# Performance work log

Measured on AMD Instinct MI355X. Metric: run time of the kernel, lower is better.

## Reference

```python
import jax, jax.numpy as jnp
import numpy as np

N, C, H, DH = 4096, 256, 8, 32
E = 32768
MAX_SPD = 3
DEG_B = 8
LN_EPS = 1e-5


def _ln(h, g, b):
    mu = jnp.mean(h, axis=-1, keepdims=True)
    var = jnp.mean((h - mu) ** 2, axis=-1, keepdims=True)
    return g * (h - mu) / jnp.sqrt(var + LN_EPS) + b


def setup_inputs() -> dict:
    key = jax.random.key(0)
    ks = jax.random.split(key, 16)
    s = 1.0 / np.sqrt(C).astype(np.float32)
    s4 = 1.0 / np.sqrt(4 * C).astype(np.float32)
    return {
        "x": jax.random.normal(ks[0], (N, C), jnp.float32),
        "edge_index": jax.random.randint(ks[1], (2, E), 0, N, dtype=jnp.int32),
        "Wq": jax.random.normal(ks[2], (C, C), jnp.float32) * s,
        "bq": jnp.zeros((C,), jnp.float32),
        "Wk": jax.random.normal(ks[3], (C, C), jnp.float32) * s,
        "bk": jnp.zeros((C,), jnp.float32),
        "Wv": jax.random.normal(ks[4], (C, C), jnp.float32) * s,
        "bv": jnp.zeros((C,), jnp.float32),
        "Wo": jax.random.normal(ks[5], (C, C), jnp.float32) * s,
        "bo": jnp.zeros((C,), jnp.float32),
        "W1": jax.random.normal(ks[6], (C, 4 * C), jnp.float32) * s,
        "b1": jnp.zeros((4 * C,), jnp.float32),
        "W2": jax.random.normal(ks[7], (4 * C, C), jnp.float32) * s4,
        "b2": jnp.zeros((C,), jnp.float32),
        "g1": jnp.ones((C,), jnp.float32),
        "beta1": jnp.zeros((C,), jnp.float32),
        "g2": jnp.ones((C,), jnp.float32),
        "beta2": jnp.zeros((C,), jnp.float32),
        # spd_emb is zero-init in torch; use small random so the bias path is exercised
        "spd_emb": jax.random.normal(ks[8], (MAX_SPD + 2, H), jnp.float32) * 0.02,
        "in_deg_emb": jax.random.normal(ks[9], (DEG_B + 1, C), jnp.float32) * 0.02,
        "out_deg_emb": jax.random.normal(ks[10], (DEG_B + 1, C), jnp.float32) * 0.02,
        "et_bias": jax.random.normal(ks[11], (), jnp.float32) * 0.02,
    }


def _bucket(d):
    # floor(log2(d+1)) clamped to [0, DEG_B]
    return jnp.clip(jnp.floor(jnp.log2(d + 1.0)), 0, DEG_B).astype(jnp.int32)


def _spd_buckets(src, dst):
    # use_reverse_spd=True: adjacency A[row=dst, col=src]; anchors = dst, probe = src.
    # Frontier F starts as identity over all nodes (superset of unique-anchor columns;
    # extra columns never probed -> identical result to torch's unique-anchor version).
    F = jnp.eye(N, dtype=jnp.float32)
    spd = jnp.full((E,), MAX_SPD + 1, dtype=jnp.int32)
    unset = jnp.ones((E,), dtype=bool)
    for k in range(1, MAX_SPD + 1):
        # (A @ F) > 0  via edge-gather + per-row max (binary reachability)
        F = (jax.ops.segment_max(F[src], dst, num_segments=N) > 0).astype(jnp.float32)
        reach = F[src, dst] > 0  # probe anchor column dst at row src
        newly = unset & reach
        spd = jnp.where(newly, k, spd)
        unset = unset & ~newly
    return jnp.clip(spd, 1, MAX_SPD + 1)


def reference(x, edge_index, Wq, bq, Wk, bk, Wv, bv, Wo, bo, W1, b1, W2, b2,
              g1, beta1, g2, beta2, spd_emb, in_deg_emb, out_deg_emb, et_bias):
    src, dst = edge_index[0], edge_index[1]
    ones = jnp.ones((E,), jnp.float32)
    in_deg = jax.ops.segment_sum(ones, dst, num_segments=N)
    out_deg = jax.ops.segment_sum(ones, src, num_segments=N)
    x_in = x + in_deg_emb[_bucket(in_deg)] + out_deg_emb[_bucket(out_deg)]

    spd = _spd_buckets(src, dst)  # [E] int in [1, MAX_SPD+1]

    xn = _ln(x_in, g1, beta1)
    Q = (xn @ Wq + bq).reshape(N, H, DH)
    K = (xn @ Wk + bk).reshape(N, H, DH)
    V = (xn @ Wv + bv).reshape(N, H, DH)

    scores = jnp.sum(Q[dst] * K[src], axis=-1) / np.sqrt(DH)  # [E, H]
    scores = scores + spd_emb[spd] + et_bias

    # segment softmax over edges sharing a destination node
    m = jax.ops.segment_max(scores, dst, num_segments=N)  # [N, H]
    m = jnp.where(jnp.isfinite(m), m, 0.0)
    e = jnp.exp(scores - m[dst])
    ssum = jax.ops.segment_sum(e, dst, num_segments=N)
    w = e / jnp.where(ssum[dst] > 0, ssum[dst], 1.0)  # [E, H]

    msg = jax.ops.segment_sum(w[:, :, None] * V[src], dst, num_segments=N)  # [N,H,DH]
    h = x_in + msg.reshape(N, C) @ Wo + bo
    hn = _ln(h, g2, beta2)
    ff = jax.nn.gelu(hn @ W1 + b1, approximate=False) @ W2 + b2
    return h + ff
```

## Files before the change

kernel.cpp:

```cpp
#include <hip/hip_runtime.h>
#include <math.h>

#define NN 4096
#define CC 256
#define HH 8
#define DHD 32
#define EE 32768
#define FW 128
#define MAXD 64

typedef float f32x4 __attribute__((ext_vector_type(4)));
typedef __bf16 bf16x8 __attribute__((ext_vector_type(8)));
typedef __bf16 bf16x4 __attribute__((ext_vector_type(4)));

__device__ __forceinline__ int bucketf(int d){
  float l = log2f((float)d + 1.0f);
  int b = (int)floorf(l);
  return b < 0 ? 0 : (b > 8 ? 8 : b);
}

__global__ void k_scatter(const int* __restrict__ src, const int* __restrict__ dst,
                          int* __restrict__ cursor, int* __restrict__ outdeg,
                          int* __restrict__ nsrc){
  int e = blockIdx.x*256+threadIdx.x;
  if(e<EE){
    int d = dst[e], s = src[e];
    atomicAdd(&outdeg[s],1);
    int p = atomicAdd(&cursor[d],1);
    if(p < MAXD) nsrc[d*MAXD+p] = s;
  }
}

__global__ void k_mid(const int* __restrict__ cursor, const int* __restrict__ nsrc,
                      unsigned* __restrict__ F1,
                      const float* __restrict__ x,
                      const int* __restrict__ outdeg, const float* __restrict__ iemb,
                      const float* __restrict__ oemb, const float* __restrict__ g,
                      const float* __restrict__ be, float* __restrict__ x_in,
                      __bf16* __restrict__ xn){
  int b = blockIdx.x;
  int tid = threadIdx.x;
  if(b < 2048){
    int d = b*2 + (tid>>7);
    int w = tid & 127;
    int cdeg = cursor[d]; if(cdeg > MAXD) cdeg = MAXD;
    const int* row = nsrc + d*MAXD;
    unsigned v = 0;
    for(int i=0;i<cdeg;i++){
      int s = row[i];
      if((s>>5) == w) v |= 1u << (s&31);
    }
    F1[(size_t)d*FW + w] = v;
    return;
  }
  int node = (b-2048)*4 + (tid >> 6);
  int lane = tid & 63;
  int bi = bucketf(cursor[node]);
  int bo = bucketf(outdeg[node]);
  float4 xv = ((const float4*)(x + (size_t)node*CC))[lane];
  float4 iv = ((const float4*)(iemb + (size_t)bi*CC))[lane];
  float4 ov = ((const float4*)(oemb + (size_t)bo*CC))[lane];
  float4 v;
  v.x = xv.x+iv.x+ov.x; v.y = xv.y+iv.y+ov.y;
  v.z = xv.z+iv.z+ov.z; v.w = xv.w+iv.w+ov.w;
  ((float4*)(x_in + (size_t)node*CC))[lane] = v;
  float s  = v.x+v.y+v.z+v.w;
  float sq = v.x*v.x+v.y*v.y+v.z*v.z+v.w*v.w;
  #pragma unroll
  for(int m=32;m>=1;m>>=1){ s += __shfl_xor(s,m); sq += __shfl_xor(sq,m); }
  float mu  = s * (1.0f/CC);
  float var = sq * (1.0f/CC) - mu*mu;
  float inv = rsqrtf(var + 1e-5f);
  float4 gv = ((const float4*)g)[lane];
  float4 bv = ((const float4*)be)[lane];
  bf16x4 o;
  o[0] = (__bf16)(gv.x*(v.x-mu)*inv + bv.x);
  o[1] = (__bf16)(gv.y*(v.y-mu)*inv + bv.y);
  o[2] = (__bf16)(gv.z*(v.z-mu)*inv + bv.z);
  o[3] = (__bf16)(gv.w*(v.w-mu)*inv + bv.w);
  *(bf16x4*)(xn + (size_t)node*CC + lane*4) = o;
}

__global__ void k_prop(const int* __restrict__ cursor, const int* __restrict__ nsrc,
                       const unsigned* __restrict__ Fin, unsigned* __restrict__ Fout){
  int d = blockIdx.x; int w = threadIdx.x;
  int cdeg = cursor[d]; if(cdeg > MAXD) cdeg = MAXD;
  const int* row = nsrc + d*MAXD;
  unsigned v = 0;
  for(int i=0;i<cdeg;i++){
    v |= Fin[(size_t)row[i]*FW + w];
  }
  Fout[(size_t)d*FW + w] = v;
}

__global__ void k_pre(const float* __restrict__ Wq, const float* __restrict__ Wk,
                      const float* __restrict__ Wv, const float* __restrict__ Wo,
                      const float* __restrict__ W1, const float* __restrict__ W2,
                      const float* __restrict__ bq, const float* __restrict__ bk,
                      const float* __restrict__ bv,
                      __bf16* __restrict__ WqkvT, __bf16* __restrict__ WoT,
                      __bf16* __restrict__ W1T, __bf16* __restrict__ W2T,
                      float* __restrict__ bqkv, int* __restrict__ zero_base){
  int b = blockIdx.x;
  int tid = threadIdx.x;
  if(b >= 193){
    zero_base[(b-193)*256 + tid] = 0;
    return;
  }
  if(b == 192){
    bqkv[tid]     = bq[tid];
    bqkv[256+tid] = bk[tid];
    bqkv[512+tid] = bv[tid];
    return;
  }
  const float* W; __bf16* Wt; int K, N, tile;
  if(b < 16)      { W=Wq; Wt=WqkvT;        K=256;  N=256;  tile=b; }
  else if(b < 32) { W=Wk; Wt=WqkvT+65536;  K=256;  N=256;  tile=b-16; }
  else if(b < 48) { W=Wv; Wt=WqkvT+131072; K=256;  N=256;  tile=b-32; }
  else if(b < 64) { W=Wo; Wt=WoT;          K=256;  N=256;  tile=b-48; }
  else if(b < 128){ W=W1; Wt=W1T;          K=256;  N=1024; tile=b-64; }
  else            { W=W2; Wt=W2T;          K=1024; N=256;  tile=b-128; }
  int nK = K/64;
  int tk = tile % nK, tn = tile / nK;
  __shared__ float T[64][65];
  int c = tid & 63, r0 = tid >> 6;
  #pragma unroll
  for(int i=0;i<16;i++){
    int row = r0*16 + i;
    T[row][c] = W[(size_t)(tk*64+row)*N + tn*64 + c];
  }
  __syncthreads();
  #pragma unroll
  for(int i=0;i<16;i++){
    int row = r0*16 + i;
    Wt[(size_t)(tn*64+row)*K + tk*64 + c] = (__bf16)T[c][row];
  }
}

template<int MODE>
__global__ __launch_bounds__(256) void k_bgemm(const __bf16* __restrict__ A, const __bf16* __restrict__ Bt,
                       const float* __restrict__ bias, const float* __restrict__ add,
                       float* __restrict__ outf, __bf16* __restrict__ outb,
                       int M, int N, int K){
  __shared__ __bf16 As[64*64];
  __shared__ __bf16 Bs[64*64];
  const int tid = threadIdx.x;
  const int lane = tid & 63;
  const int w = tid >> 6;
  const int wr = w >> 1, wc = w & 1;
  const int l15 = lane & 15, g = lane >> 4;
  const int bm = blockIdx.y*64, bn = blockIdx.x*64;
  f32x4 acc[2][2] = {};
  for(int k0=0; k0<K; k0+=64){
    #pragma unroll
    for(int rep=0; rep<2; rep++){
      int q = tid + rep*256;
      int row = q>>3;
      int scb = ((q&7)*16) ^ ((row&7)<<4);
      const __bf16* srcA = A  + (size_t)(bm+row)*K + k0 + (scb>>1);
      const __bf16* srcB = Bt + (size_t)(bn+row)*K + k0 + (scb>>1);
      __builtin_amdgcn_global_load_lds(
        (const __attribute__((address_space(1))) void*)srcA,
        (__attribute__((address_space(3))) void*)((char*)As + q*16), 16, 0, 0);
      __builtin_amdgcn_global_load_lds(
        (const __attribute__((address_space(1))) void*)srcB,
        (__attribute__((address_space(3))) void*)((char*)Bs + q*16), 16, 0, 0);
    }
    __syncthreads();
    #pragma unroll
    for(int ks=0; ks<2; ks++){
      bf16x8 a[2], b[2];
      #pragma unroll
      for(int i=0;i<2;i++){
        int row = wr*32 + i*16 + l15;
        int byte_ = row*128 + ks*64 + g*16; byte_ ^= (row&7)<<4;
        a[i] = *(const bf16x8*)((const char*)As + byte_);
      }
      #pragma unroll
      for(int j=0;j<2;j++){
        int row = wc*32 + j*16 + l15;
        int byte_ = row*128 + ks*64 + g*16; byte_ ^= (row&7)<<4;
        b[j] = *(const bf16x8*)((const char*)Bs + byte_);
      }
      #pragma unroll
      for(int i=0;i<2;i++)
        #pragma unroll
        for(int j=0;j<2;j++)
          acc[i][j] = __builtin_amdgcn_mfma_f32_16x16x32_bf16(a[i], b[j], acc[i][j], 0, 0, 0);
    }
    __syncthreads();
  }
  #pragma unroll
  for(int i=0;i<2;i++){
    #pragma unroll
    for(int j=0;j<2;j++){
      int col = bn + wc*32 + j*16 + l15;
      float bv = bias[col];
      #pragma unroll
      for(int r=0;r<4;r++){
        int rowg = bm + wr*32 + i*16 + g*4 + r;
        float v = acc[i][j][r] + bv;
        if(MODE==1) v += add[(size_t)rowg*N + col];
        if(MODE==2){
          v = 0.5f*v*(1.0f + erff(v*0.70710678118654752f));
          outb[(size_t)rowg*N + col] = (__bf16)v;
        } else if(MODE==3){
          outb[(size_t)rowg*N + col] = (__bf16)v;
        } else {
          outf[(size_t)rowg*N + col] = v;
        }
      }
    }
  }
}

__global__ __launch_bounds__(256) void k_wln(const __bf16* __restrict__ A, const __bf16* __restrict__ Bt,
                    const float* __restrict__ bias, const float* __restrict__ add,
                    const float* __restrict__ g2, const float* __restrict__ be2,
                    float* __restrict__ hbuf, __bf16* __restrict__ hn){
  __shared__ __bf16 As[16*64];
  __shared__ __bf16 Bs[256*64];
  __shared__ float partS[64], partQ[64], muv[16], invv[16];
  const int tid = threadIdx.x;
  const int lane = tid & 63;
  const int w = tid >> 6;
  const int l15 = lane & 15, g = lane >> 4;
  const int bm = blockIdx.x*16;
  const int K = 256, N = 256;
  f32x4 acc[4] = {};
  for(int k0=0; k0<K; k0+=64){
    if(tid < 128){
      int q = tid;
      int row = q>>3;
      int scb = ((q&7)*16) ^ ((row&7)<<4);
      const __bf16* srcA = A + (size_t)(bm+row)*K + k0 + (scb>>1);
      __builtin_amdgcn_global_load_lds(
        (const __attribute__((address_space(1))) void*)srcA,
        (__attribute__((address_space(3))) void*)((char*)As + q*16), 16, 0, 0);
    }
    #pragma unroll
    for(int rep=0; rep<8; rep++){
      int q = tid + rep*256;
      int row = q>>3;
      int scb = ((q&7)*16) ^ ((row&7)<<4);
      const __bf16* srcB = Bt + (size_t)row*K + k0 + (scb>>1);
      __builtin_amdgcn_global_load_lds(
        (const __attribute__((address_space(1))) void*)srcB,
        (__attribute__((address_space(3))) void*)((char*)Bs + q*16), 16, 0, 0);
    }
    __syncthreads();
    #pragma unroll
    for(int ks=0; ks<2; ks++){
      bf16x8 a, b[4];
      { int row = l15;
        int byte_ = row*128 + ks*64 + g*16; byte_ ^= (row&7)<<4;
        a = *(const bf16x8*)((const char*)As + byte_); }
      #pragma unroll
      for(int j=0;j<4;j++){
        int row = w*64 + j*16 + l15;
        int byte_ = row*128 + ks*64 + g*16; byte_ ^= (row&7)<<4;
        b[j] = *(const bf16x8*)((const char*)Bs + byte_);
      }
      #pragma unroll
      for(int j=0;j<4;j++)
        acc[j] = __builtin_amdgcn_mfma_f32_16x16x32_bf16(a, b[j], acc[j], 0, 0, 0);
    }
    __syncthreads();
  }
  float v[4][4];
  #pragma unroll
  for(int j=0;j<4;j++){
    int col = w*64 + j*16 + l15;
    float bv = bias[col];
    #pragma unroll
    for(int r=0;r<4;r++){
      int rowg = bm + g*4 + r;
      v[j][r] = acc[j][r] + bv + add[(size_t)rowg*N + col];
    }
  }
  float s[4], qq[4];
  #pragma unroll
  for(int r=0;r<4;r++){
    s[r] = v[0][r]+v[1][r]+v[2][r]+v[3][r];
    qq[r] = v[0][r]*v[0][r]+v[1][r]*v[1][r]+v[2][r]*v[2][r]+v[3][r]*v[3][r];
  }
  #pragma unroll
  for(int m=8;m>=1;m>>=1){
    #pragma unroll
    for(int r=0;r<4;r++){ s[r] += __shfl_xor(s[r],m); qq[r] += __shfl_xor(qq[r],m); }
  }
  if(l15==0){
    #pragma unroll
    for(int r=0;r<4;r++){ partS[w*16 + g*4 + r] = s[r]; partQ[w*16 + g*4 + r] = qq[r]; }
  }
  __syncthreads();
  if(tid < 16){
    float S = partS[tid] + partS[16+tid] + partS[32+tid] + partS[48+tid];
    float Q = partQ[tid] + partQ[16+tid] + partQ[32+tid] + partQ[48+tid];
    float mu = S * (1.0f/256.0f);
    float var = Q * (1.0f/256.0f) - mu*mu;
    muv[tid] = mu;
    invv[tid] = rsqrtf(var + 1e-5f);
  }
  __syncthreads();
  #pragma unroll
  for(int j=0;j<4;j++){
    int col = w*64 + j*16 + l15;
    float gv = g2[col], bev = be2[col];
    #pragma unroll
    for(int r=0;r<4;r++){
      int rowg = bm + g*4 + r;
      float mu = muv[g*4+r], iv = invv[g*4+r];
      hbuf[(size_t)rowg*N + col] = v[j][r];
      hn[(size_t)rowg*N + col] = (__bf16)(gv*(v[j][r]-mu)*iv + bev);
    }
  }
}

__global__ __launch_bounds__(256) void k_pq(const int* __restrict__ cursor, const int* __restrict__ nsrc,
                    const unsigned* __restrict__ F2, unsigned* __restrict__ F3,
                    const __bf16* __restrict__ A, const __bf16* __restrict__ Bt,
                    const float* __restrict__ bias, __bf16* __restrict__ outb){
  __shared__ __bf16 As[64*64];
  __shared__ __bf16 Bs[64*64];
  const int b = blockIdx.x;
  const int tid = threadIdx.x;
  if(b < 2048){
    int d = b*2 + (tid>>7);
    int w_ = tid & 127;
    int cdeg = cursor[d]; if(cdeg > MAXD) cdeg = MAXD;
    const int* row = nsrc + d*MAXD;
    unsigned v = 0;
    for(int i=0;i<cdeg;i++) v |= F2[(size_t)row[i]*FW + w_];
    F3[(size_t)d*FW + w_] = v;
    return;
  }
  const int bx = b - 2048;
  const int N = 768, K = 256;
  const int bm = (bx/12)*64, bn = (bx%12)*64;
  const int lane = tid & 63;
  const int w = tid >> 6;
  const int wr = w >> 1, wc = w & 1;
  const int l15 = lane & 15, g = lane >> 4;
  f32x4 acc[2][2] = {};
  for(int k0=0; k0<K; k0+=64){
    #pragma unroll
    for(int rep=0; rep<2; rep++){
      int q = tid + rep*256;
      int row = q>>3;
      int scb = ((q&7)*16) ^ ((row&7)<<4);
      const __bf16* srcA = A  + (size_t)(bm+row)*K + k0 + (scb>>1);
      const __bf16* srcB = Bt + (size_t)(bn+row)*K + k0 + (scb>>1);
      __builtin_amdgcn_global_load_lds(
        (const __attribute__((address_space(1))) void*)srcA,
        (__attribute__((address_space(3))) void*)((char*)As + q*16), 16, 0, 0);
      __builtin_amdgcn_global_load_lds(
        (const __attribute__((address_space(1))) void*)srcB,
        (__attribute__((address_space(3))) void*)((char*)Bs + q*16), 16, 0, 0);
    }
    __syncthreads();
    #pragma unroll
    for(int ks=0; ks<2; ks++){
      bf16x8 a[2], bb[2];
      #pragma unroll
      for(int i=0;i<2;i++){
        int row = wr*32 + i*16 + l15;
        int byte_ = row*128 + ks*64 + g*16; byte_ ^= (row&7)<<4;
        a[i] = *(const bf16x8*)((const char*)As + byte_);
      }
      #pragma unroll
      for(int j=0;j<2;j++){
        int row = wc*32 + j*16 + l15;
        int byte_ = row*128 + ks*64 + g*16; byte_ ^= (row&7)<<4;
        bb[j] = *(const bf16x8*)((const char*)Bs + byte_);
      }
      #pragma unroll
      for(int i=0;i<2;i++)
        #pragma unroll
        for(int j=0;j<2;j++)
          acc[i][j] = __builtin_amdgcn_mfma_f32_16x16x32_bf16(a[i], bb[j], acc[i][j], 0, 0, 0);
    }
    __syncthreads();
  }
  #pragma unroll
  for(int i=0;i<2;i++){
    #pragma unroll
    for(int j=0;j<2;j++){
      int col = bn + wc*32 + j*16 + l15;
      float bv = bias[col];
      #pragma unroll
      for(int r=0;r<4;r++){
        int rowg = bm + wr*32 + i*16 + g*4 + r;
        outb[(size_t)rowg*N + col] = (__bf16)(acc[i][j][r] + bv);
      }
    }
  }
}

__global__ void k_sagg(const int* __restrict__ nsrc, const int* __restrict__ cursor,
                       const __bf16* __restrict__ QKV,
                       const unsigned* __restrict__ F1, const unsigned* __restrict__ F2,
                       const unsigned* __restrict__ F3,
                       const float* __restrict__ spde, __bf16* __restrict__ msg){
  __shared__ float scs[MAXD][9];
  __shared__ int   sl[MAXD];
  __shared__ int   spi[MAXD];
  const int d = blockIdx.x;
  const int t = threadIdx.x;
  int deg = cursor[d]; if(deg > MAXD) deg = MAXD;
  if(t < deg){
    int s = nsrc[d*MAXD+t];
    sl[t] = s;
    size_t wi = (size_t)s*FW + (d>>5); unsigned bb = 1u << (d&31);
    int sp = 4;
    if(F3[wi] & bb) sp = 3;
    if(F2[wi] & bb) sp = 2;
    if(F1[wi] & bb) sp = 1;
    spi[t] = sp;
  }
  __syncthreads();
  { const int i0 = t>>5, h = (t>>2)&7, q = t&3;
    bf16x8 qv = *(const bf16x8*)(QKV + (size_t)d*768 + h*DHD + q*8);
    for(int i=i0; i<deg; i+=8){
      bf16x8 kv = *(const bf16x8*)(QKV + (size_t)sl[i]*768 + 256 + h*DHD + q*8);
      float p = 0.f;
      #pragma unroll
      for(int u=0;u<8;u++) p += (float)qv[u] * (float)kv[u];
      p += __shfl_xor(p,1);
      p += __shfl_xor(p,2);
      if(q==0) scs[i][h] = p * 0.17677669529663687f + spde[spi[i]*HH + h];
    }
  }
  __syncthreads();
  { const int h = t >> 5, l = t & 31;
    float m = -3.0e38f;
    for(int i=l;i<deg;i+=32) m = fmaxf(m, scs[i][h]);
    #pragma unroll
    for(int mk=16;mk>=1;mk>>=1) m = fmaxf(m, __shfl_xor(m,mk));
    float ss = 0.f;
    for(int i=l;i<deg;i+=32) ss += expf(scs[i][h]-m);
    #pragma unroll
    for(int mk=16;mk>=1;mk>>=1) ss += __shfl_xor(ss,mk);
    float inv = (ss>0.f) ? 1.f/ss : 1.f;
    for(int i=l;i<deg;i+=32) scs[i][h] = expf(scs[i][h]-m)*inv;
  }
  __syncthreads();
  { const int h = t >> 5, c = t & 31;
    float acc = 0.f;
    for(int i=0;i<deg;i++)
      acc += scs[i][h] * (float)QKV[(size_t)sl[i]*768 + 512 + h*DHD + c];
    msg[(size_t)d*CC + h*DHD + c] = (__bf16)acc;
  }
}

extern "C" void kernel_launch(void* const* d_in, const int* in_sizes, int n_in,
                              void* d_out, int out_size, void* d_ws, size_t ws_size,
                              hipStream_t stream){
  const float* x  = (const float*)d_in[0];
  const int*  ei  = (const int*)d_in[1];
  const float* Wq = (const float*)d_in[2];  const float* bq = (const float*)d_in[3];
  const float* Wk = (const float*)d_in[4];  const float* bk = (const float*)d_in[5];
  const float* Wv = (const float*)d_in[6];  const float* bv = (const float*)d_in[7];
  const float* Wo = (const float*)d_in[8];  const float* bo = (const float*)d_in[9];
  const float* W1 = (const float*)d_in[10]; const float* b1 = (const float*)d_in[11];
  const float* W2 = (const float*)d_in[12]; const float* b2 = (const float*)d_in[13];
  const float* g1 = (const float*)d_in[14]; const float* be1= (const float*)d_in[15];
  const float* g2 = (const float*)d_in[16]; const float* be2= (const float*)d_in[17];
  const float* spde = (const float*)d_in[18];
  const float* iemb = (const float*)d_in[19];
  const float* oemb = (const float*)d_in[20];
  const float* etb  = (const float*)d_in[21]; (void)etb;
  const int* src = ei;
  const int* dst = ei + EE;
  float* out = (float*)d_out;

  const size_t NC = (size_t)NN*CC;
  float* ws   = (float*)d_ws;
  float* x_in = ws;
  float* hbuf = ws + NC;
  int* cursor = (int*)(ws + 2*NC);
  int* outdeg = cursor + NN;
  unsigned* F1 = (unsigned*)(ws + 2*NC + 12288);
  unsigned* F2 = F1 + (size_t)NN*FW;
  unsigned* F3 = F2 + (size_t)NN*FW;
  __bf16* QKV  = (__bf16*)(F3 + (size_t)NN*FW);
  int* nsrc    = (int*)(ws + 5255168);
  __bf16* xn_bf  = (__bf16*)(ws + 5517312);
  __bf16* msg_bf = (__bf16*)(ws + 6041600);
  __bf16* WqkvT  = (__bf16*)(ws + 6565888);
  __bf16* WoT    = WqkvT + 196608;
  __bf16* W1T    = WoT + 65536;
  __bf16* W2T    = W1T + 262144;
  float* bqkv    = ws + 6959104;
  __bf16* ff1_bf = (__bf16*)(ws + 2*NC);
  __bf16* hn_bf  = (__bf16*)(ws + 4*NC);

  k_pre<<<225,256,0,stream>>>(Wq,Wk,Wv,Wo,W1,W2,bq,bk,bv,WqkvT,WoT,W1T,W2T,bqkv,cursor);
  k_scatter<<<EE/256,256,0,stream>>>(src,dst,cursor,outdeg,nsrc);
  k_mid<<<3072,256,0,stream>>>(cursor,nsrc,F1,x,outdeg,iemb,oemb,g1,be1,x_in,xn_bf);
  k_prop<<<NN,FW,0,stream>>>(cursor,nsrc,F1,F2);
  k_pq<<<2816,256,0,stream>>>(cursor,nsrc,F2,F3,xn_bf,WqkvT,bqkv,QKV);
  k_sagg<<<NN,256,0,stream>>>(nsrc,cursor,QKV,F1,F2,F3,spde,msg_bf);
  k_wln<<<NN/16,256,0,stream>>>(msg_bf, WoT, bo, x_in, g2, be2, hbuf, hn_bf);
  dim3 gf1(1024/64, NN/64);
  k_bgemm<2><<<gf1,256,0,stream>>>(hn_bf, W1T, b1, nullptr, nullptr, ff1_bf, NN, 1024, 256);
  dim3 gf2(256/64, NN/64);
  k_bgemm<1><<<gf2,256,0,stream>>>(ff1_bf, W2T, b2, hbuf, out, nullptr, NN, 256, 1024);
}
```

Measured before the change: 80.71 us.

## Drop third frontier propagation; compute hop-3 reachability on demand per edge

Removes the separate k_prop launch and the full F3 bitset frontier. The F2 propagation now runs inside k_pq alongside the QKV GEMM. The aggregation kernel decides distance 3 lazily: for edges not at distance 1 or 2, it scans the source's neighbors' F2 bits. This saves one kernel launch and a full N×N bitset pass, but adds divergent per-thread loops over neighbor lists in k_sagg for far edges.

Measured after the change: 90.84 us. 12.5% more time.

```diff
diff --git a/kernel.cpp b/kernel.cpp
--- a/kernel.cpp
+++ b/kernel.cpp
@@ -79,18 +79,6 @@
   o[2] = (__bf16)(gv.z*(v.z-mu)*inv + bv.z);
   o[3] = (__bf16)(gv.w*(v.w-mu)*inv + bv.w);
   *(bf16x4*)(xn + (size_t)node*CC + lane*4) = o;
-}
-
-__global__ void k_prop(const int* __restrict__ cursor, const int* __restrict__ nsrc,
-                       const unsigned* __restrict__ Fin, unsigned* __restrict__ Fout){
-  int d = blockIdx.x; int w = threadIdx.x;
-  int cdeg = cursor[d]; if(cdeg > MAXD) cdeg = MAXD;
-  const int* row = nsrc + d*MAXD;
-  unsigned v = 0;
-  for(int i=0;i<cdeg;i++){
-    v |= Fin[(size_t)row[i]*FW + w];
-  }
-  Fout[(size_t)d*FW + w] = v;
 }
 
 __global__ void k_pre(const float* __restrict__ Wq, const float* __restrict__ Wk,
@@ -318,7 +306,7 @@
 }
 
 __global__ __launch_bounds__(256) void k_pq(const int* __restrict__ cursor, const int* __restrict__ nsrc,
-                    const unsigned* __restrict__ F2, unsigned* __restrict__ F3,
+                    const unsigned* __restrict__ F1, unsigned* __restrict__ F2,
                     const __bf16* __restrict__ A, const __bf16* __restrict__ Bt,
                     const float* __restrict__ bias, __bf16* __restrict__ outb){
   __shared__ __bf16 As[64*64];
@@ -331,8 +319,8 @@
     int cdeg = cursor[d]; if(cdeg > MAXD) cdeg = MAXD;
     const int* row = nsrc + d*MAXD;
     unsigned v = 0;
-    for(int i=0;i<cdeg;i++) v |= F2[(size_t)row[i]*FW + w_];
-    F3[(size_t)d*FW + w_] = v;
+    for(int i=0;i<cdeg;i++) v |= F1[(size_t)row[i]*FW + w_];
+    F2[(size_t)d*FW + w_] = v;
     return;
   }
   const int bx = b - 2048;
@@ -400,7 +388,6 @@
 __global__ void k_sagg(const int* __restrict__ nsrc, const int* __restrict__ cursor,
                        const __bf16* __restrict__ QKV,
                        const unsigned* __restrict__ F1, const unsigned* __restrict__ F2,
-                       const unsigned* __restrict__ F3,
                        const float* __restrict__ spde, __bf16* __restrict__ msg){
   __shared__ float scs[MAXD][9];
   __shared__ int   sl[MAXD];
@@ -411,11 +398,18 @@
   if(t < deg){
     int s = nsrc[d*MAXD+t];
     sl[t] = s;
-    size_t wi = (size_t)s*FW + (d>>5); unsigned bb = 1u << (d&31);
-    int sp = 4;
-    if(F3[wi] & bb) sp = 3;
-    if(F2[wi] & bb) sp = 2;
-    if(F1[wi] & bb) sp = 1;
+    const int wo = d>>5; const unsigned bb = 1u << (d&31);
+    int sp;
+    if(F1[(size_t)s*FW + wo] & bb) sp = 1;
+    else if(F2[(size_t)s*FW + wo] & bb) sp = 2;
+    else {
+      sp = 4;
+      int sdeg = cursor[s]; if(sdeg > MAXD) sdeg = MAXD;
+      const int* srow = nsrc + s*MAXD;
+      for(int i=0;i<sdeg;i++){
+        if(F2[(size_t)srow[i]*FW + wo] & bb){ sp = 3; break; }
+      }
+    }
     spi[t] = sp;
   }
   __syncthreads();
@@ -482,8 +476,7 @@
   int* outdeg = cursor + NN;
   unsigned* F1 = (unsigned*)(ws + 2*NC + 12288);
   unsigned* F2 = F1 + (size_t)NN*FW;
-  unsigned* F3 = F2 + (size_t)NN*FW;
-  __bf16* QKV  = (__bf16*)(F3 + (size_t)NN*FW);
+  __bf16* QKV  = (__bf16*)(ws + 3682304);
   int* nsrc    = (int*)(ws + 5255168);
   __bf16* xn_bf  = (__bf16*)(ws + 5517312);
   __bf16* msg_bf = (__bf16*)(ws + 6041600);
@@ -498,9 +491,8 @@
   k_pre<<<225,256,0,stream>>>(Wq,Wk,Wv,Wo,W1,W2,bq,bk,bv,WqkvT,WoT,W1T,W2T,bqkv,cursor);
   k_scatter<<<EE/256,256,0,stream>>>(src,dst,cursor,outdeg,nsrc);
   k_mid<<<3072,256,0,stream>>>(cursor,nsrc,F1,x,outdeg,iemb,oemb,g1,be1,x_in,xn_bf);
-  k_prop<<<NN,FW,0,stream>>>(cursor,nsrc,F1,F2);
-  k_pq<<<2816,256,0,stream>>>(cursor,nsrc,F2,F3,xn_bf,WqkvT,bqkv,QKV);
-  k_sagg<<<NN,256,0,stream>>>(nsrc,cursor,QKV,F1,F2,F3,spde,msg_bf);
+  k_pq<<<2816,256,0,stream>>>(cursor,nsrc,F1,F2,xn_bf,WqkvT,bqkv,QKV);
+  k_sagg<<<NN,256,0,stream>>>(nsrc,cursor,QKV,F1,F2,spde,msg_bf);
   k_wln<<<NN/16,256,0,stream>>>(msg_bf, WoT, bo, x_in, g2, be2, hbuf, hn_bf);
   dim3 gf1(1024/64, NN/64);
   k_bgemm<2><<<gf1,256,0,stream>>>(hn_bf, W1T, b1, nullptr, nullptr, ff1_bf, NN, 1024, 256);
```
